# Kernel tuning notes

Measured on AMD Instinct MI355X. Metric: run time of the kernel, lower is better.

## Reference

```python
import jax, jax.numpy as jnp
import numpy as np
import math

# Model config (see init_kwargs)
E = 1024   # emb_size
H = 8      # ffwd_num_head
D = 128    # ffwd_head_size (E == H*D)
NE = 16    # ffwd_num_expert
A = 2      # ffwd_num_expert_active
S = 256    # ffwd_expert_size
B = 2      # batch_size_fwd
T = 2048   # context_window
NUM_BLOCK = 12


def setup_inputs() -> dict:
    key = jax.random.key(0)
    ks = jax.random.split(key, 5)
    x = jax.random.normal(ks[0], (B, T, E), jnp.float32)
    # fc_in_fused: Linear(E, 4E+NE, bias=False), torch weight shape (out,in)
    w_in = 0.02 * jax.random.normal(ks[1], (4 * E + NE, E), jnp.float32)
    # fc_out_fused: Linear(2E, E), std 0.02/sqrt(num_block)
    w_out = (0.02 / math.sqrt(NUM_BLOCK)) * jax.random.normal(ks[2], (E, 2 * E), jnp.float32)
    # k_ffwd/v_ffwd: original (1,H,NE*S,D); stored here as (NE,H,S,D) for per-expert scan
    k_ffwd = 0.02 * jax.random.normal(ks[3], (NE, H, S, D), jnp.float32)
    v_ffwd = 0.02 * jax.random.normal(ks[4], (NE, H, S, D), jnp.float32)
    return {"x": x, "w_in": w_in, "w_out": w_out, "k_ffwd": k_ffwd, "v_ffwd": v_ffwd}


def _rope(t):
    # Standard half-split RoPE, base 10000. t: (B,T,H,D)
    half = t.shape[-1] // 2
    inv_freq = 1.0 / (10000.0 ** (jnp.arange(half, dtype=jnp.float32) / half))
    ang = jnp.arange(t.shape[1], dtype=jnp.float32)[:, None] * inv_freq  # (T, half)
    cos = jnp.cos(ang)[None, :, None, :]
    sin = jnp.sin(ang)[None, :, None, :]
    t1, t2 = t[..., :half], t[..., half:]
    return jnp.concatenate([t1 * cos - t2 * sin, t1 * sin + t2 * cos], axis=-1)


def reference(x, w_in, w_out, k_ffwd, v_ffwd):
    Bx, Tx, _ = x.shape
    h = x @ w_in.T  # (B,T,4E+NE)
    q_f, q_a, k_a, v_a, router_logits = jnp.split(h, [E, 2 * E, 3 * E, 4 * E], axis=-1)

    # top-k routing (order of the k slots is irrelevant: outputs are summed)
    gate_logits, assign = jax.lax.top_k(router_logits, A)  # (B,T,A)
    gate = jax.nn.sigmoid(gate_logits)

    # --- attention half: causal softmax attention, scale 1/sqrt(D), with RoPE ---
    q = _rope(q_a.reshape(Bx, Tx, H, D))
    k = _rope(k_a.reshape(Bx, Tx, H, D))
    v = v_a.reshape(Bx, Tx, H, D)
    scores = jnp.einsum('bqhd,bkhd->bhqk', q, k) / math.sqrt(D)
    causal = jnp.tril(jnp.ones((Tx, Tx), dtype=bool))
    scores = jnp.where(causal, scores, -jnp.inf)
    p = jax.nn.softmax(scores, axis=-1)
    attn_out = jnp.einsum('bhqk,bkhd->bqhd', p, v).reshape(Bx, Tx, E)

    # --- MoE-FFN half, expressed as attention with score_mod log1p(gelu):
    # exp(lse)*softmax recovers sum_s (1+gelu(q.k_s)) v_s; subtracting sum_s v_s
    # leaves sum_s gelu(q.k_s) v_s over the assigned expert's slots. ---
    qf = q_f.reshape(Bx, Tx, H, D)

    def step(acc, ekv):
        e, ke, ve = ekv  # ke, ve: (H,S,D)
        s = jnp.einsum('bthd,hsd->bths', qf, ke)
        a = jax.nn.gelu(s, approximate=False)  # torch F.gelu default = exact erf
        o = jnp.einsum('bths,hsd->bthd', a, ve)
        g = jnp.sum(jnp.where(assign == e, gate, 0.0), axis=-1)  # (B,T)
        return acc + g[..., None, None] * o, None

    acc0 = jnp.zeros((Bx, Tx, H, D), x.dtype)
    ffwd_out, _ = jax.lax.scan(step, acc0, (jnp.arange(NE), k_ffwd, v_ffwd))
    ffwd_out = ffwd_out.reshape(Bx, Tx, E)

    out = jnp.concatenate([attn_out, ffwd_out], axis=-1) @ w_out.T  # (B,T,E)
    return out
```

## Files before the change

### kernel.cpp

```cpp
#include <hip/hip_runtime.h>
#include <hip/hip_bf16.h>
#include <math.h>

#define E 1024
#define NHP 4096
#define NEXP 16
#define HH 8
#define DD 128
#define SS 256
#define BB 2
#define TT 2048
#define BT 4096

typedef __attribute__((ext_vector_type(8))) short bf16x8;
typedef __attribute__((ext_vector_type(4))) float f32x4;

#define GLDS16(g, s) __builtin_amdgcn_global_load_lds( \
    (const __attribute__((address_space(1))) void*)(g), \
    (__attribute__((address_space(3))) void*)(s), 16, 0, 0)

__device__ __forceinline__ ushort f2b(float f) {
    union { float f; unsigned u; } v; v.f = f;
    unsigned r = (v.u + 0x7FFFu + ((v.u >> 16) & 1u)) >> 16;
    return (ushort)r;
}
__device__ __forceinline__ float b2f(ushort u) {
    union { unsigned u; float f; } v; v.u = ((unsigned)u) << 16;
    return v.f;
}
__device__ __forceinline__ float gelu_fast(float x) {
    float u2 = x * x;
    float tu = x * (1.5957691216f + 0.0713548163f * u2);
    float e = __expf(tu);
    float sig = 1.f - __builtin_amdgcn_rcpf(e + 1.f);
    return x * sig;
}

__global__ void cvtk_swz(const float* __restrict__ in, ushort* __restrict__ outp,
                         int kshift, int n)
{
    int i = (blockIdx.x * blockDim.x + threadIdx.x) * 8;
    if (i >= n) return;
    int row = i >> kshift;
    int colb = (i - (row << kshift)) * 2;
    float4 f0 = *(const float4*)(in + i);
    float4 f1 = *(const float4*)(in + i + 4);
    ushort4 u0, u1;
    u0.x = f2b(f0.x); u0.y = f2b(f0.y); u0.z = f2b(f0.z); u0.w = f2b(f0.w);
    u1.x = f2b(f1.x); u1.y = f2b(f1.y); u1.z = f2b(f1.z); u1.w = f2b(f1.w);
    char* dst = (char*)outp + ((size_t)row << (kshift + 1)) + (colb ^ ((row & 7) << 4));
    *(ushort4*)dst = u0;
    *(ushort4*)(dst + 8) = u1;
}

template<int BF16OUT>
__global__ __launch_bounds__(256) void gemm_bf16(
    const ushort* __restrict__ A, int lda,
    const ushort* __restrict__ B, int ldb,
    void* __restrict__ Cv, int ldc, int K)
{
    __shared__ ushort As[128 * 64];
    __shared__ ushort Bs[128 * 64];
    const int t = threadIdx.x;
    const int l = t & 63, w = t >> 6;
    const int m0 = blockIdx.y * 128, n0 = blockIdx.x * 128;
    const int wr = w >> 1, wc = w & 1;
    const int fr = l & 15, fg = l >> 4;

    const int srow = w * 32 + (l >> 3);
    const int sboff = (l & 7) * 16;
    const char* Ag = (const char*)A + ((size_t)(m0 + srow) * lda) * 2 + sboff;
    const char* Bg = (const char*)B + ((size_t)(n0 + srow) * ldb) * 2 + sboff;
    const int aswz = (fr & 7) << 4;

    f32x4 acc[4][4];
    #pragma unroll
    for (int i = 0; i < 4; ++i)
        #pragma unroll
        for (int j = 0; j < 4; ++j) { acc[i][j][0]=0.f; acc[i][j][1]=0.f; acc[i][j][2]=0.f; acc[i][j][3]=0.f; }

    for (int k0b = 0; k0b < K * 2; k0b += 128) {
        #pragma unroll
        for (int i = 0; i < 4; ++i) {
            GLDS16(Ag + (size_t)(i * 8) * lda * 2 + k0b, (char*)As + (w * 32 + i * 8) * 128);
            GLDS16(Bg + (size_t)(i * 8) * ldb * 2 + k0b, (char*)Bs + (w * 32 + i * 8) * 128);
        }
        __syncthreads();
        #pragma unroll
        for (int ksub = 0; ksub < 2; ++ksub) {
            bf16x8 a[4], b[4];
            #pragma unroll
            for (int mi = 0; mi < 4; ++mi)
                a[mi] = *(const bf16x8*)((const char*)As + (wr * 64 + mi * 16 + fr) * 128 + ((ksub * 64 + fg * 16) ^ aswz));
            #pragma unroll
            for (int ni = 0; ni < 4; ++ni)
                b[ni] = *(const bf16x8*)((const char*)Bs + (wc * 64 + ni * 16 + fr) * 128 + ((ksub * 64 + fg * 16) ^ aswz));
            #pragma unroll
            for (int mi = 0; mi < 4; ++mi)
                #pragma unroll
                for (int ni = 0; ni < 4; ++ni)
                    acc[mi][ni] = __builtin_amdgcn_mfma_f32_16x16x32_bf16(a[mi], b[ni], acc[mi][ni], 0, 0, 0);
        }
        __syncthreads();
    }
    #pragma unroll
    for (int mi = 0; mi < 4; ++mi)
        #pragma unroll
        for (int ni = 0; ni < 4; ++ni) {
            const int row = m0 + wr * 64 + mi * 16 + fg * 4;
            const int col = n0 + wc * 64 + ni * 16 + fr;
            #pragma unroll
            for (int r = 0; r < 4; ++r) {
                if (BF16OUT)
                    ((ushort*)Cv)[(size_t)(row + r) * ldc + col] = f2b(acc[mi][ni][r]);
                else
                    ((float*)Cv)[(size_t)(row + r) * ldc + col] = acc[mi][ni][r];
            }
        }
}

__global__ __launch_bounds__(256) void router_logits(
    const float* __restrict__ x, const float* __restrict__ w_in,
    float* __restrict__ gval, int* __restrict__ eidx, ushort* __restrict__ xb)
{
    const int m = blockIdx.x * 4 + (threadIdx.x >> 6);
    const int lane = threadIdx.x & 63;

    const float* xp = x + (size_t)m * 1024 + lane * 4;
    float4 xv0 = *(const float4*)(xp);
    float4 xv1 = *(const float4*)(xp + 256);
    float4 xv2 = *(const float4*)(xp + 512);
    float4 xv3 = *(const float4*)(xp + 768);

    {
        const int swrow = (m & 7) << 4;
        char* xrow = (char*)xb + (size_t)m * 2048;
        ushort4 u;
        u.x = f2b(xv0.x); u.y = f2b(xv0.y); u.z = f2b(xv0.z); u.w = f2b(xv0.w);
        *(ushort4*)(xrow + ((lane * 8 + 0 * 512) ^ swrow)) = u;
        u.x = f2b(xv1.x); u.y = f2b(xv1.y); u.z = f2b(xv1.z); u.w = f2b(xv1.w);
        *(ushort4*)(xrow + ((lane * 8 + 1 * 512) ^ swrow)) = u;
        u.x = f2b(xv2.x); u.y = f2b(xv2.y); u.z = f2b(xv2.z); u.w = f2b(xv2.w);
        *(ushort4*)(xrow + ((lane * 8 + 2 * 512) ^ swrow)) = u;
        u.x = f2b(xv3.x); u.y = f2b(xv3.y); u.z = f2b(xv3.z); u.w = f2b(xv3.w);
        *(ushort4*)(xrow + ((lane * 8 + 3 * 512) ^ swrow)) = u;
    }

    float p[16];
    #pragma unroll
    for (int e = 0; e < 16; ++e) {
        const float* wp = w_in + (size_t)(4096 + e) * 1024 + lane * 4;
        float4 w0 = *(const float4*)(wp);
        float4 w1 = *(const float4*)(wp + 256);
        float4 w2 = *(const float4*)(wp + 512);
        float4 w3 = *(const float4*)(wp + 768);
        float s0 = xv0.x * w0.x + xv0.y * w0.y + xv0.z * w0.z + xv0.w * w0.w;
        float s1 = xv1.x * w1.x + xv1.y * w1.y + xv1.z * w1.z + xv1.w * w1.w;
        float s2 = xv2.x * w2.x + xv2.y * w2.y + xv2.z * w2.z + xv2.w * w2.w;
        float s3 = xv3.x * w3.x + xv3.y * w3.y + xv3.z * w3.z + xv3.w * w3.w;
        p[e] = (s0 + s1) + (s2 + s3);
    }
    #pragma unroll
    for (int d = 1; d < 64; d <<= 1) {
        #pragma unroll
        for (int e = 0; e < 16; ++e)
            p[e] += __shfl_xor(p[e], d);
    }
    float best = -1e30f; int bi = 0;
    #pragma unroll
    for (int e = 0; e < 16; ++e)
        if (p[e] > best) { best = p[e]; bi = e; }
    float best2 = -1e30f; int bi2 = 0;
    #pragma unroll
    for (int e = 0; e < 16; ++e)
        if (e != bi && p[e] > best2) { best2 = p[e]; bi2 = e; }

    if (lane == 0) {
        gval[m * 2 + 0] = 1.f / (1.f + __expf(-best));
        gval[m * 2 + 1] = 1.f / (1.f + __expf(-best2));
        eidx[m * 2 + 0] = bi;
        eidx[m * 2 + 1] = bi2;
    }
}

__global__ __launch_bounds__(256) void build_lists(
    const int* __restrict__ eidx,
    int* __restrict__ counts, int* __restrict__ plist)
{
    const int e = blockIdx.x;
    const int t = threadIdx.x;
    const int w = t >> 6, lane = t & 63;
    __shared__ int wbase[4];
    __shared__ int running;
    if (t == 0) running = 0;
    __syncthreads();
    for (int c = 0; c < 2 * BT; c += 256) {
        const int p = c + t;
        const bool match = (eidx[p] == e);
        unsigned long long mask = __ballot(match);
        int lpre = __popcll(mask & ((lane == 63) ? 0x7FFFFFFFFFFFFFFFull
                                                 : ((1ull << lane) - 1ull)));
        if (lane == 0) wbase[w] = __popcll(mask);
        __syncthreads();
        int pre = running;
        #pragma unroll
        for (int i = 0; i < 4; ++i) if (i < w) pre += wbase[i];
        const int tot = wbase[0] + wbase[1] + wbase[2] + wbase[3];
        if (match) plist[e * BT + pre + lpre] = p;
        __syncthreads();
        if (t == 0) running += tot;
        __syncthreads();
    }
    if (t == 0) counts[e] = running;
}

__global__ void rope2(const ushort* __restrict__ hb,
                      ushort* __restrict__ qb, ushort* __restrict__ kb)
{
    int m = blockIdx.x;
    int t = threadIdx.x;
    int hd = t >> 6, j = t & 63;
    int tok = m & 2047, b = m >> 11;
    float invf = __expf(-(float)j * (9.210340371976184f / 64.f));
    float ang = (float)tok * invf;
    float s, c;
    sincosf(ang, &s, &c);
    const ushort* base = hb + (size_t)m * NHP + E + hd * DD;
    float q1 = b2f(base[j]), q2 = b2f(base[j + 64]);
    float k1 = b2f(base[E + j]), k2 = b2f(base[E + j + 64]);
    float qa = q1 * c - q2 * s, qbv = q1 * s + q2 * c;
    float ka = k1 * c - k2 * s, kbv = k1 * s + k2 * c;
    size_t rowb = ((size_t)(b * 8 + hd) * 2048 + tok) * 256;
    int sw = (tok & 7) << 4;
    *(ushort*)((char*)qb + rowb + ((2 * j) ^ sw))        = f2b(qa);
    *(ushort*)((char*)qb + rowb + ((2 * (j + 64)) ^ sw)) = f2b(qbv);
    *(ushort*)((char*)kb + rowb + ((2 * j) ^ sw))        = f2b(ka);
    *(ushort*)((char*)kb + rowb + ((2 * (j + 64)) ^ sw)) = f2b(kbv);
}

__global__ __launch_bounds__(256) void vtrans(const ushort* __restrict__ hb,
                                              ushort* __restrict__ vtb)
{
    __shared__ ushort T[64][132];
    int bh = blockIdx.y, ck = blockIdx.x;
    int b = bh >> 3, hd = bh & 7;
    int t = threadIdx.x;
    int tok0 = ck * 64;
    #pragma unroll
    for (int it = 0; it < 8; ++it) {
        int idx = it * 256 + t, r = idx >> 5, c4 = idx & 31;
        ushort4 f = *(const ushort4*)(hb + (size_t)(b * 2048 + tok0 + r) * NHP + 3 * E + hd * DD + c4 * 4);
        T[r][c4 * 4 + 0] = f.x; T[r][c4 * 4 + 1] = f.y;
        T[r][c4 * 4 + 2] = f.z; T[r][c4 * 4 + 3] = f.w;
    }
    __syncthreads();
    int g = t >> 4, fr = t & 15;
    #pragma unroll
    for (int dd = 0; dd < 8; ++dd) {
        int d = g + dd * 16;
        ushort4 u;
        u.x = T[4 * fr + 0][d]; u.y = T[4 * fr + 1][d];
        u.z = T[4 * fr + 2][d]; u.w = T[4 * fr + 3][d];
        size_t ob = ((size_t)(bh * 128 + d) * 2048 + tok0) * 2;
        *(ushort4*)((char*)vtb + ob + ((8 * fr) ^ ((d & 7) << 4))) = u;
    }
}

__global__ __launch_bounds__(256) void cvt_kv(
    const float* __restrict__ kf, const float* __restrict__ vf,
    ushort* __restrict__ kfb, ushort* __restrict__ vtf)
{
    __shared__ float T[64][132];
    int eh = blockIdx.y, st = blockIdx.x;
    int s0 = st * 64;
    int t = threadIdx.x;
    const float* kbp = kf + (size_t)eh * SS * DD + (size_t)s0 * DD;
    const float* vbp = vf + (size_t)eh * SS * DD + (size_t)s0 * DD;
    for (int i = t; i < 64 * 32; i += 256) {
        int r = i >> 5, c4 = i & 31;
        float4 f = *(const float4*)(kbp + (size_t)r * DD + c4 * 4);
        ushort4 u;
        u.x = f2b(f.x); u.y = f2b(f.y); u.z = f2b(f.z); u.w = f2b(f.w);
        *(ushort4*)((char*)kfb + ((size_t)eh * 256 + s0 + r) * 256 + ((c4 * 8) ^ ((r & 7) << 4))) = u;
    }
    for (int i = t; i < 64 * 32; i += 256) {
        int r = i >> 5, c4 = i & 31;
        float4 f = *(const float4*)(vbp + (size_t)r * DD + c4 * 4);
        T[r][c4 * 4 + 0] = f.x; T[r][c4 * 4 + 1] = f.y;
        T[r][c4 * 4 + 2] = f.z; T[r][c4 * 4 + 3] = f.w;
    }
    __syncthreads();
    int g = t >> 4, fr = t & 15;
    #pragma unroll
    for (int dd = 0; dd < 8; ++dd) {
        int d = g + dd * 16;
        ushort4 u;
        u.x = f2b(T[4 * fr + 0][d]); u.y = f2b(T[4 * fr + 1][d]);
        u.z = f2b(T[4 * fr + 2][d]); u.w = f2b(T[4 * fr + 3][d]);
        size_t ob = ((size_t)eh * 128 + d) * 512 + s0 * 2;
        *(ushort4*)((char*)vtf + ob + ((8 * fr) ^ ((d & 7) << 4))) = u;
    }
}

__global__ __launch_bounds__(512, 1) void attn_mfma(
    const ushort* __restrict__ qb, const ushort* __restrict__ kb,
    const ushort* __restrict__ vtb, ushort* __restrict__ catb)
{
    __shared__ ushort Ks[2][128 * 128];
    __shared__ ushort Vs[2][128 * 128];
    __shared__ ushort Ps[8][16 * 72];
    __shared__ float  LlS[8][16];

    const int t = threadIdx.x, l = t & 63, w = t >> 6;
    const int fr = l & 15, fg = l >> 4;
    const int wl = w & 3, hh = w >> 2;
    const int lin = blockIdx.x;
    const int bh = (lin & 7) * 2 + (lin >> 7);
    const int tpair = (lin >> 3) & 15;
    const int swz = (fr & 7) << 4;
    ushort* Pw = (ushort*)Ps[w];

    #pragma unroll 1
    for (int pass = 0; pass < 2; ++pass) {
        const int qt = pass ? (31 - tpair) : tpair;
        const int qbase = qt * 64;
        const int nkt = (qt + 2) >> 1;
        const int qg = qbase + wl * 16 + fg * 4;

        bf16x8 qreg[4];
        {
            const char* qrow = (const char*)qb + ((size_t)(bh * 2048 + qbase + wl * 16 + fr)) * 256;
            #pragma unroll
            for (int ks = 0; ks < 4; ++ks)
                qreg[ks] = *(const bf16x8*)(qrow + ((ks * 64 + fg * 16) ^ swz));
        }
        {
            const char* ksrc = (const char*)kb + ((size_t)(bh * 2048 + w * 16)) * 256;
            const char* vsrc = (const char*)vtb + ((size_t)(bh * 128 + w * 16)) * 4096;
            #pragma unroll
            for (int i = 0; i < 4; ++i) {
                GLDS16(ksrc + (size_t)(i * 4 + (l >> 4)) * 256 + (l & 15) * 16,
                       (char*)Ks[0] + (w * 16 + i * 4) * 256);
                GLDS16(vsrc + (size_t)(i * 4 + (l >> 4)) * 4096 + (l & 15) * 16,
                       (char*)Vs[0] + (w * 16 + i * 4) * 256);
            }
        }

        f32x4 po[8];
        #pragma unroll
        for (int i = 0; i < 8; ++i) { po[i][0]=0.f; po[i][1]=0.f; po[i][2]=0.f; po[i][3]=0.f; }
        float lrow[4] = {0.f, 0.f, 0.f, 0.f};

        asm volatile("s_waitcnt vmcnt(0)" ::: "memory");
        __syncthreads();

        for (int kt = 0; kt < nkt; ++kt) {
            const int cur = kt & 1;
            if (kt + 1 < nkt) {
                const int kvn = (kt + 1) * 128;
                const char* ksrc = (const char*)kb + ((size_t)(bh * 2048 + kvn + w * 16)) * 256;
                const char* vsrc = (const char*)vtb + ((size_t)(bh * 128 + w * 16)) * 4096 + kvn * 2;
                #pragma unroll
                for (int i = 0; i < 4; ++i) {
                    GLDS16(ksrc + (size_t)(i * 4 + (l >> 4)) * 256 + (l & 15) * 16,
                           (char*)Ks[cur ^ 1] + (w * 16 + i * 4) * 256);
                    GLDS16(vsrc + (size_t)(i * 4 + (l >> 4)) * 4096 + (l & 15) * 16,
                           (char*)Vs[cur ^ 1] + (w * 16 + i * 4) * 256);
                }
            }
            const int kvb = kt * 128;

            f32x4 s[4];
            #pragma unroll
            for (int i = 0; i < 4; ++i) { s[i][0]=0.f; s[i][1]=0.f; s[i][2]=0.f; s[i][3]=0.f; }
            __builtin_amdgcn_s_setprio(1);
            #pragma unroll
            for (int ks = 0; ks < 4; ++ks) {
                #pragma unroll
                for (int fn = 0; fn < 4; ++fn) {
                    const int brow = hh * 64 + fn * 16 + fr;
                    bf16x8 bb = *(const bf16x8*)((const char*)Ks[cur] + brow * 256 + ((ks * 64 + fg * 16) ^ swz));
                    s[fn] = __builtin_amdgcn_mfma_f32_16x16x32_bf16(qreg[ks], bb, s[fn], 0, 0, 0);
                }
            }
            __builtin_amdgcn_s_setprio(0);

            const int colbase = kvb + hh * 64;
            const bool needmask = (colbase + 64 > qbase + wl * 16);
            float ps[4] = {0.f, 0.f, 0.f, 0.f};
            #pragma unroll
            for (int fn = 0; fn < 4; ++fn)
                #pragma unroll
                for (int r = 0; r < 4; ++r) {
                    float v = s[fn][r] * 0.08838834764831845f;
                    bool masked = needmask && (colbase + fn * 16 + fr > qg + r);
                    float p = masked ? 0.f : __expf(v);
                    ps[r] += p;
                    Pw[(fg * 4 + r) * 72 + fn * 16 + fr] = f2b(p);
                }
            #pragma unroll
            for (int r = 0; r < 4; ++r) {
                float s2 = ps[r];
                s2 += __shfl_xor(s2, 1);
                s2 += __shfl_xor(s2, 2);
                s2 += __shfl_xor(s2, 4);
                s2 += __shfl_xor(s2, 8);
                lrow[r] += s2;
            }

            asm volatile("s_waitcnt lgkmcnt(0)" ::: "memory");
            __builtin_amdgcn_sched_barrier(0);

            __builtin_amdgcn_s_setprio(1);
            #pragma unroll
            for (int ks2 = 0; ks2 < 2; ++ks2) {
                bf16x8 pa = *(const bf16x8*)((const char*)Pw + fr * 144 + ks2 * 64 + fg * 16);
                #pragma unroll
                for (int fn2 = 0; fn2 < 8; ++fn2) {
                    const int vrow = fn2 * 16 + fr;
                    bf16x8 bv = *(const bf16x8*)((const char*)Vs[cur] + vrow * 256 + ((hh * 128 + ks2 * 64 + fg * 16) ^ swz));
                    po[fn2] = __builtin_amdgcn_mfma_f32_16x16x32_bf16(pa, bv, po[fn2], 0, 0, 0);
                }
            }
            __builtin_amdgcn_s_setprio(0);

            asm volatile("s_waitcnt vmcnt(0)" ::: "memory");
            __syncthreads();
        }

        if (fr == 0) {
            #pragma unroll
            for (int r = 0; r < 4; ++r)
                LlS[w][fg * 4 + r] = lrow[r];
        }
        __syncthreads();
        float linv[4];
        #pragma unroll
        for (int r = 0; r < 4; ++r)
            linv[r] = 1.f / (lrow[r] + LlS[w ^ 4][fg * 4 + r]);
        float* PO = (float*)&Ks[0][0];
        if (hh == 1) {
            #pragma unroll
            for (int fn2 = 0; fn2 < 8; ++fn2)
                #pragma unroll
                for (int r = 0; r < 4; ++r)
                    PO[(wl * 16 + fg * 4 + r) * 128 + fn2 * 16 + fr] = po[fn2][r];
        }
        __syncthreads();
        if (hh == 0) {
            const int mg = (bh >> 3) * 2048 + qbase + wl * 16 + fg * 4;
            #pragma unroll
            for (int r = 0; r < 4; ++r) {
                const int rswz = ((mg + r) & 7) << 4;
                #pragma unroll
                for (int fn2 = 0; fn2 < 8; ++fn2) {
                    float v = po[fn2][r] + PO[(wl * 16 + fg * 4 + r) * 128 + fn2 * 16 + fr];
                    int colb = ((bh & 7) * 128 + fn2 * 16 + fr) * 2;
                    *(ushort*)((char*)catb + (size_t)(mg + r) * 4096 + (colb ^ rswz)) = f2b(v * linv[r]);
                }
            }
        }
        __syncthreads();
    }
}

__global__ __launch_bounds__(256, 1) void ffn_mfma2(
    const ushort* __restrict__ hb,
    const float* __restrict__ gv,
    const int* __restrict__ counts,
    const int* __restrict__ plist,
    const ushort* __restrict__ kfb, const ushort* __restrict__ vtf,
    ushort* __restrict__ pairout)
{
    __shared__ ushort Ks[256 * 128];
    __shared__ ushort Vs[128 * 256];
    __shared__ ushort Qs[64 * 128];
    __shared__ ushort Ps[4][16 * 72];

    const int t = threadIdx.x, l = t & 63, w = t >> 6;
    const int fr = l & 15, fg = l >> 4;
    const int half = blockIdx.x, hd = blockIdx.y, e = blockIdx.z;
    const int eh = e * HH + hd;
    const int n_e = counts[e];

    {
        const char* kbase = (const char*)kfb + (size_t)eh * 65536;
        const char* vbase = (const char*)vtf + (size_t)eh * 65536;
        #pragma unroll
        for (int i = 0; i < 16; ++i) {
            GLDS16(kbase + (w * 64 + i * 4) * 256 + l * 16, (char*)Ks + (w * 64 + i * 4) * 256);
            GLDS16(vbase + w * 16384 + i * 1024 + l * 16, (char*)Vs + w * 16384 + i * 1024);
        }
    }
    __syncthreads();

    const int arow = w * 16 + fr;
    const int aswz = (arow & 7) << 4;
    ushort* Pw = (ushort*)Ps[w];
    const int rl4 = l >> 4;
    const int lb = (l & 15) * 16;

    for (int tb = half * 64; tb < n_e; tb += 128) {
        #pragma unroll
        for (int i = 0; i < 4; ++i) {
            int row = w * 16 + i * 4 + rl4;
            int gr = tb + row;
            int p = plist[e * BT + min(gr, n_e - 1)];
            int m = p >> 1;
            const char* src = (const char*)hb + (size_t)m * 8192 + hd * 256 + (lb ^ ((row & 7) << 4));
            GLDS16(src, (char*)Qs + (w * 16 + i * 4) * 256);
        }
        asm volatile("s_waitcnt vmcnt(0)" ::: "memory");

        f32x4 po[8];
        #pragma unroll
        for (int i = 0; i < 8; ++i) { po[i][0]=0.f; po[i][1]=0.f; po[i][2]=0.f; po[i][3]=0.f; }

        #pragma unroll
        for (int kt = 0; kt < 4; ++kt) {
            const int kvb = kt * 64;
            f32x4 sA[4];
            #pragma unroll
            for (int i = 0; i < 4; ++i) { sA[i][0]=0.f; sA[i][1]=0.f; sA[i][2]=0.f; sA[i][3]=0.f; }
            #pragma unroll
            for (int ks = 0; ks < 4; ++ks) {
                bf16x8 aa = *(const bf16x8*)((const char*)Qs + arow * 256 + ((ks * 64 + fg * 16) ^ aswz));
                #pragma unroll
                for (int fn = 0; fn < 4; ++fn) {
                    const int brow = kvb + fn * 16 + fr;
                    bf16x8 bb = *(const bf16x8*)((const char*)Ks + brow * 256 + ((ks * 64 + fg * 16) ^ ((brow & 7) << 4)));
                    sA[fn] = __builtin_amdgcn_mfma_f32_16x16x32_bf16(aa, bb, sA[fn], 0, 0, 0);
                }
            }
            #pragma unroll
            for (int fn = 0; fn < 4; ++fn)
                #pragma unroll
                for (int r = 0; r < 4; ++r)
                    Pw[(fg * 4 + r) * 72 + fn * 16 + fr] = f2b(gelu_fast(sA[fn][r]));
            asm volatile("s_waitcnt lgkmcnt(0)" ::: "memory");
            #pragma unroll
            for (int ks2 = 0; ks2 < 2; ++ks2) {
                bf16x8 pa = *(const bf16x8*)((const char*)Pw + fr * 144 + ks2 * 64 + fg * 16);
                #pragma unroll
                for (int fn2 = 0; fn2 < 8; ++fn2) {
                    const int vrow = fn2 * 16 + fr;
                    bf16x8 bv = *(const bf16x8*)((const char*)Vs + vrow * 512 + kt * 128 + ((ks2 * 64 + fg * 16) ^ ((vrow & 7) << 4)));
                    po[fn2] = __builtin_amdgcn_mfma_f32_16x16x32_bf16(pa, bv, po[fn2], 0, 0, 0);
                }
            }
        }
        const int rloc = w * 16 + fg * 4;
        #pragma unroll
        for (int r = 0; r < 4; ++r) {
            int gr = tb + rloc + r;
            if (gr < n_e) {
                int p = plist[e * BT + gr];
                float g = gv[p];
                #pragma unroll
                for (int fn2 = 0; fn2 < 8; ++fn2)
                    pairout[(size_t)p * 1024 + hd * DD + fn2 * 16 + fr] = f2b(g * po[fn2][r]);
            }
        }
    }
}

__global__ void combine_kernel(const ushort* __restrict__ po, ushort* __restrict__ catb)
{
    int i = blockIdx.x * blockDim.x + threadIdx.x;
    if (i >= BT * 128) return;
    int m = i >> 7, c = i & 127;
    const ushort* a = po + (size_t)(2 * m) * 1024 + c * 8;
    const ushort* b = po + (size_t)(2 * m + 1) * 1024 + c * 8;
    ushort4 a0 = *(const ushort4*)a, a1 = *(const ushort4*)(a + 4);
    ushort4 b0 = *(const ushort4*)b, b1 = *(const ushort4*)(b + 4);
    ushort4 o0, o1;
    o0.x = f2b(b2f(a0.x) + b2f(b0.x)); o0.y = f2b(b2f(a0.y) + b2f(b0.y));
    o0.z = f2b(b2f(a0.z) + b2f(b0.z)); o0.w = f2b(b2f(a0.w) + b2f(b0.w));
    o1.x = f2b(b2f(a1.x) + b2f(b1.x)); o1.y = f2b(b2f(a1.y) + b2f(b1.y));
    o1.z = f2b(b2f(a1.z) + b2f(b1.z)); o1.w = f2b(b2f(a1.w) + b2f(b1.w));
    char* dst = (char*)catb + (size_t)m * 4096 + 2048 + ((c * 16) ^ ((m & 7) << 4));
    *(ushort4*)dst = o0;
    *(ushort4*)(dst + 8) = o1;
}

extern "C" void kernel_launch(void* const* d_in, const int* in_sizes, int n_in,
                              void* d_out, int out_size, void* d_ws, size_t ws_size,
                              hipStream_t stream)
{
    const float* x     = (const float*)d_in[0];
    const float* w_in  = (const float*)d_in[1];
    const float* w_out = (const float*)d_in[2];
    const float* kf    = (const float*)d_in[3];
    const float* vf    = (const float*)d_in[4];
    float* out = (float*)d_out;

    char* W = (char*)d_ws;
    ushort* hb      = (ushort*)(W + 0);
    ushort* xb      = (ushort*)(W + 33554432);
    ushort* wib     = (ushort*)(W + 41943040);
    ushort* kfb     = xb;
    ushort* vtf     = wib;
    ushort* wob     = (ushort*)(W + 50331648);
    ushort* qb2     = (ushort*)(W + 54525952);
    ushort* kb2     = (ushort*)(W + 62914560);
    ushort* vtb     = (ushort*)(W + 71303168);
    ushort* catb    = (ushort*)(W + 79691776);
    ushort* pairout = (ushort*)(W + 96468992);
    float*  gv      = (float*)(W + 113246208);
    int*    counts  = (int*)(W + 113278976);
    int*    plist   = (int*)(W + 113279040);
    int*    eidx    = (int*)(W + 113541184);

    cvtk_swz<<<2048, 256, 0, stream>>>(w_in, wib, 10, 4096 * 1024);
    cvtk_swz<<<1024, 256, 0, stream>>>(w_out, wob, 11, 1024 * 2048);

    router_logits<<<BT / 4, 256, 0, stream>>>(x, w_in, gv, eidx, xb);
    build_lists<<<NEXP, 256, 0, stream>>>(eidx, counts, plist);

    gemm_bf16<1><<<dim3(32, 32), 256, 0, stream>>>(xb, 1024, wib, 1024, hb, NHP, 1024);

    rope2<<<BT, 512, 0, stream>>>(hb, qb2, kb2);
    vtrans<<<dim3(32, 16), 256, 0, stream>>>(hb, vtb);
    cvt_kv<<<dim3(4, NEXP * HH), 256, 0, stream>>>(kf, vf, kfb, vtf);

    attn_mfma<<<dim3(256), 512, 0, stream>>>(qb2, kb2, vtb, catb);

    ffn_mfma2<<<dim3(2, HH, NEXP), 256, 0, stream>>>(hb, gv, counts, plist, kfb, vtf, pairout);
    combine_kernel<<<2048, 256, 0, stream>>>(pairout, catb);

    gemm_bf16<0><<<dim3(8, 32), 256, 0, stream>>>(catb, 2048, wob, 2048, out, 1024, 2048);
}
```

Baseline: 239.6 us.

## Fuse RoPE and V transpose into the input projection GEMM epilogue

Replaces the generic input-projection GEMM plus the separate rope2 and vtrans kernels with one GEMM whose epilogue picks a path by output column region. The q_f columns go to a compact buffer, the q/k columns get RoPE applied through shared memory before being written in swizzled layout, and the v columns are written directly in transposed layout. This removes two kernel launches and the write and reread of the full 4096-wide intermediate. The cost is a heavier epilogue with sincos per element and scattered 8-byte transposed stores.

Result: faster. 234.1 us (median of 2 runs) (-2.3%).

```diff
diff --git a/kernel.cpp b/kernel.cpp
--- a/kernel.cpp
+++ b/kernel.cpp
@@ -3,7 +3,6 @@
 #include <math.h>
 
 #define E 1024
-#define NHP 4096
 #define NEXP 16
 #define HH 8
 #define DD 128
@@ -117,6 +116,131 @@
                     ((float*)Cv)[(size_t)(row + r) * ldc + col] = acc[mi][ni][r];
             }
         }
+}
+
+__global__ __launch_bounds__(256) void gemm1_fused(
+    const ushort* __restrict__ A, const ushort* __restrict__ B,
+    ushort* __restrict__ hbq,
+    ushort* __restrict__ qb, ushort* __restrict__ kb,
+    ushort* __restrict__ vtb)
+{
+    __shared__ ushort sh[128 * 128];
+    ushort* As = sh;
+    ushort* Bs = sh + 128 * 64;
+    const int t = threadIdx.x;
+    const int l = t & 63, w = t >> 6;
+    const int m0 = blockIdx.y * 128, n0 = blockIdx.x * 128;
+    const int wr = w >> 1, wc = w & 1;
+    const int fr = l & 15, fg = l >> 4;
+
+    const int srow = w * 32 + (l >> 3);
+    const int sboff = (l & 7) * 16;
+    const char* Ag = (const char*)A + ((size_t)(m0 + srow) * 1024) * 2 + sboff;
+    const char* Bg = (const char*)B + ((size_t)(n0 + srow) * 1024) * 2 + sboff;
+    const int aswz = (fr & 7) << 4;
+
+    f32x4 acc[4][4];
+    #pragma unroll
+    for (int i = 0; i < 4; ++i)
+        #pragma unroll
+        for (int j = 0; j < 4; ++j) { acc[i][j][0]=0.f; acc[i][j][1]=0.f; acc[i][j][2]=0.f; acc[i][j][3]=0.f; }
+
+    for (int k0b = 0; k0b < 2048; k0b += 128) {
+        #pragma unroll
+        for (int i = 0; i < 4; ++i) {
+            GLDS16(Ag + (size_t)(i * 8) * 2048 + k0b, (char*)As + (w * 32 + i * 8) * 128);
+            GLDS16(Bg + (size_t)(i * 8) * 2048 + k0b, (char*)Bs + (w * 32 + i * 8) * 128);
+        }
+        __syncthreads();
+        #pragma unroll
+        for (int ksub = 0; ksub < 2; ++ksub) {
+            bf16x8 a[4], b[4];
+            #pragma unroll
+            for (int mi = 0; mi < 4; ++mi)
+                a[mi] = *(const bf16x8*)((const char*)As + (wr * 64 + mi * 16 + fr) * 128 + ((ksub * 64 + fg * 16) ^ aswz));
+            #pragma unroll
+            for (int ni = 0; ni < 4; ++ni)
+                b[ni] = *(const bf16x8*)((const char*)Bs + (wc * 64 + ni * 16 + fr) * 128 + ((ksub * 64 + fg * 16) ^ aswz));
+            #pragma unroll
+            for (int mi = 0; mi < 4; ++mi)
+                #pragma unroll
+                for (int ni = 0; ni < 4; ++ni)
+                    acc[mi][ni] = __builtin_amdgcn_mfma_f32_16x16x32_bf16(a[mi], b[ni], acc[mi][ni], 0, 0, 0);
+        }
+        __syncthreads();
+    }
+
+    const int region = blockIdx.x >> 3;
+    const int hd = blockIdx.x & 7;
+
+    if (region == 0) {
+        #pragma unroll
+        for (int mi = 0; mi < 4; ++mi)
+            #pragma unroll
+            for (int ni = 0; ni < 4; ++ni) {
+                const int row = m0 + wr * 64 + mi * 16 + fg * 4;
+                const int col = n0 + wc * 64 + ni * 16 + fr;
+                #pragma unroll
+                for (int r = 0; r < 4; ++r)
+                    hbq[(size_t)(row + r) * 1024 + col] = f2b(acc[mi][ni][r]);
+            }
+    } else if (region == 3) {
+        #pragma unroll
+        for (int mi = 0; mi < 4; ++mi) {
+            const int rowg = m0 + wr * 64 + mi * 16 + fg * 4;
+            const int tok = rowg & 2047, bt = rowg >> 11;
+            const int bh = bt * 8 + hd;
+            #pragma unroll
+            for (int ni = 0; ni < 4; ++ni) {
+                const int d = wc * 64 + ni * 16 + fr;
+                ushort4 u;
+                u.x = f2b(acc[mi][ni][0]); u.y = f2b(acc[mi][ni][1]);
+                u.z = f2b(acc[mi][ni][2]); u.w = f2b(acc[mi][ni][3]);
+                char* dst = (char*)vtb + (size_t)(bh * 128 + d) * 4096
+                          + (tok >> 6) * 128 + ((2 * (tok & 63)) ^ ((d & 7) << 4));
+                *(ushort4*)dst = u;
+            }
+        }
+    } else {
+        #pragma unroll
+        for (int mi = 0; mi < 4; ++mi)
+            #pragma unroll
+            for (int ni = 0; ni < 4; ++ni) {
+                const int rl = wr * 64 + mi * 16 + fg * 4;
+                const int cl = wc * 64 + ni * 16 + fr;
+                #pragma unroll
+                for (int r = 0; r < 4; ++r)
+                    sh[(rl + r) * 128 + cl] = f2b(acc[mi][ni][r]);
+            }
+        __syncthreads();
+        ushort* outb = (region == 1) ? qb : kb;
+        #pragma unroll
+        for (int it = 0; it < 4; ++it) {
+            const int item = it * 256 + t;
+            const int rloc = item >> 3, g = item & 7;
+            const int rowg = m0 + rloc;
+            const int tok = rowg & 2047, bt = rowg >> 11;
+            const int sw = (tok & 7) << 4;
+            char* rowbase = (char*)outb + ((size_t)((bt * 8 + hd) * 2048 + tok)) * 256;
+            ushort lo[8], hi[8];
+            #pragma unroll
+            for (int jj = 0; jj < 8; ++jj) {
+                const int j = g * 8 + jj;
+                float t1 = b2f(sh[rloc * 128 + j]);
+                float t2 = b2f(sh[rloc * 128 + 64 + j]);
+                float invf = __expf(-(float)j * (9.210340371976184f / 64.f));
+                float ang = (float)tok * invf;
+                float s, c;
+                sincosf(ang, &s, &c);
+                lo[jj] = f2b(t1 * c - t2 * s);
+                hi[jj] = f2b(t1 * s + t2 * c);
+            }
+            *(ushort4*)(rowbase + ((16 * g) ^ sw))        = *(ushort4*)&lo[0];
+            *(ushort4*)(rowbase + (((16 * g) ^ sw) + 8))  = *(ushort4*)&lo[4];
+            *(ushort4*)(rowbase + ((16 * g + 128) ^ sw))       = *(ushort4*)&hi[0];
+            *(ushort4*)(rowbase + (((16 * g + 128) ^ sw) + 8)) = *(ushort4*)&hi[4];
+        }
+    }
 }
 
 __global__ __launch_bounds__(256) void router_logits(
@@ -214,58 +338,6 @@
     if (t == 0) counts[e] = running;
 }
 
-__global__ void rope2(const ushort* __restrict__ hb,
-                      ushort* __restrict__ qb, ushort* __restrict__ kb)
-{
-    int m = blockIdx.x;
-    int t = threadIdx.x;
-    int hd = t >> 6, j = t & 63;
-    int tok = m & 2047, b = m >> 11;
-    float invf = __expf(-(float)j * (9.210340371976184f / 64.f));
-    float ang = (float)tok * invf;
-    float s, c;
-    sincosf(ang, &s, &c);
-    const ushort* base = hb + (size_t)m * NHP + E + hd * DD;
-    float q1 = b2f(base[j]), q2 = b2f(base[j + 64]);
-    float k1 = b2f(base[E + j]), k2 = b2f(base[E + j + 64]);
-    float qa = q1 * c - q2 * s, qbv = q1 * s + q2 * c;
-    float ka = k1 * c - k2 * s, kbv = k1 * s + k2 * c;
-    size_t rowb = ((size_t)(b * 8 + hd) * 2048 + tok) * 256;
-    int sw = (tok & 7) << 4;
-    *(ushort*)((char*)qb + rowb + ((2 * j) ^ sw))        = f2b(qa);
-    *(ushort*)((char*)qb + rowb + ((2 * (j + 64)) ^ sw)) = f2b(qbv);
-    *(ushort*)((char*)kb + rowb + ((2 * j) ^ sw))        = f2b(ka);
-    *(ushort*)((char*)kb + rowb + ((2 * (j + 64)) ^ sw)) = f2b(kbv);
-}
-
-__global__ __launch_bounds__(256) void vtrans(const ushort* __restrict__ hb,
-                                              ushort* __restrict__ vtb)
-{
-    __shared__ ushort T[64][132];
-    int bh = blockIdx.y, ck = blockIdx.x;
-    int b = bh >> 3, hd = bh & 7;
-    int t = threadIdx.x;
-    int tok0 = ck * 64;
-    #pragma unroll
-    for (int it = 0; it < 8; ++it) {
-        int idx = it * 256 + t, r = idx >> 5, c4 = idx & 31;
-        ushort4 f = *(const ushort4*)(hb + (size_t)(b * 2048 + tok0 + r) * NHP + 3 * E + hd * DD + c4 * 4);
-        T[r][c4 * 4 + 0] = f.x; T[r][c4 * 4 + 1] = f.y;
-        T[r][c4 * 4 + 2] = f.z; T[r][c4 * 4 + 3] = f.w;
-    }
-    __syncthreads();
-    int g = t >> 4, fr = t & 15;
-    #pragma unroll
-    for (int dd = 0; dd < 8; ++dd) {
-        int d = g + dd * 16;
-        ushort4 u;
-        u.x = T[4 * fr + 0][d]; u.y = T[4 * fr + 1][d];
-        u.z = T[4 * fr + 2][d]; u.w = T[4 * fr + 3][d];
-        size_t ob = ((size_t)(bh * 128 + d) * 2048 + tok0) * 2;
-        *(ushort4*)((char*)vtb + ob + ((8 * fr) ^ ((d & 7) << 4))) = u;
-    }
-}
-
 __global__ __launch_bounds__(256) void cvt_kv(
     const float* __restrict__ kf, const float* __restrict__ vf,
     ushort* __restrict__ kfb, ushort* __restrict__ vtf)
@@ -465,7 +537,7 @@
 }
 
 __global__ __launch_bounds__(256, 1) void ffn_mfma2(
-    const ushort* __restrict__ hb,
+    const ushort* __restrict__ hbq,
     const float* __restrict__ gv,
     const int* __restrict__ counts,
     const int* __restrict__ plist,
@@ -507,7 +579,7 @@
             int gr = tb + row;
             int p = plist[e * BT + min(gr, n_e - 1)];
             int m = p >> 1;
-            const char* src = (const char*)hb + (size_t)m * 8192 + hd * 256 + (lb ^ ((row & 7) << 4));
+            const char* src = (const char*)hbq + (size_t)m * 2048 + hd * 256 + (lb ^ ((row & 7) << 4));
             GLDS16(src, (char*)Qs + (w * 16 + i * 4) * 256);
         }
         asm volatile("s_waitcnt vmcnt(0)" ::: "memory");
@@ -595,7 +667,7 @@
     float* out = (float*)d_out;
 
     char* W = (char*)d_ws;
-    ushort* hb      = (ushort*)(W + 0);
+    ushort* hbq     = (ushort*)(W + 0);
     ushort* xb      = (ushort*)(W + 33554432);
     ushort* wib     = (ushort*)(W + 41943040);
     ushort* kfb     = xb;
@@ -617,15 +689,13 @@
     router_logits<<<BT / 4, 256, 0, stream>>>(x, w_in, gv, eidx, xb);
     build_lists<<<NEXP, 256, 0, stream>>>(eidx, counts, plist);
 
-    gemm_bf16<1><<<dim3(32, 32), 256, 0, stream>>>(xb, 1024, wib, 1024, hb, NHP, 1024);
-
-    rope2<<<BT, 512, 0, stream>>>(hb, qb2, kb2);
-    vtrans<<<dim3(32, 16), 256, 0, stream>>>(hb, vtb);
+    gemm1_fused<<<dim3(32, 32), 256, 0, stream>>>(xb, wib, hbq, qb2, kb2, vtb);
+
     cvt_kv<<<dim3(4, NEXP * HH), 256, 0, stream>>>(kf, vf, kfb, vtf);
 
     attn_mfma<<<dim3(256), 512, 0, stream>>>(qb2, kb2, vtb, catb);
 
-    ffn_mfma2<<<dim3(2, HH, NEXP), 256, 0, stream>>>(hb, gv, counts, plist, kfb, vtf, pairout);
+    ffn_mfma2<<<dim3(2, HH, NEXP), 256, 0, stream>>>(hbq, gv, counts, plist, kfb, vtf, pairout);
     combine_kernel<<<2048, 256, 0, stream>>>(pairout, catb);
 
     gemm_bf16<0><<<dim3(8, 32), 256, 0, stream>>>(catb, 2048, wob, 2048, out, 1024, 2048);
```
